# Optimization experiments

Measured on AMD Instinct MI355X. Metric: run time of the kernel, lower is better.

Reference implementation:

```python
import jax, jax.numpy as jnp
import numpy as np

EMBED_DIM = 256
N_HEADS = 1
NORM_FACTOR = float(np.sqrt(EMBED_DIM / N_HEADS))


def setup_inputs() -> dict:
    key = jax.random.key(0)
    ks = jax.random.split(key, 7)
    B, S, E = 4, 4096, EMBED_DIM
    scale = 1.0 / np.sqrt(E)
    x = jax.random.normal(ks[0], (B, S, E), dtype=jnp.float32)
    Wq = jax.random.normal(ks[1], (E, E), dtype=jnp.float32) * scale
    bq = jax.random.normal(ks[2], (E,), dtype=jnp.float32) * 0.01
    Wk = jax.random.normal(ks[3], (E, E), dtype=jnp.float32) * scale
    bk = jax.random.normal(ks[4], (E,), dtype=jnp.float32) * 0.01
    Wv = jax.random.normal(ks[5], (E, E), dtype=jnp.float32) * scale
    bv = jax.random.normal(ks[6], (E,), dtype=jnp.float32) * 0.01
    return {"x": x, "Wq": Wq, "bq": bq, "Wk": Wk, "bk": bk, "Wv": Wv, "bv": bv}


def reference(x, Wq, bq, Wk, bk, Wv, bv):
    # Linear projections (torch Linear: x @ W.T + b; W here stored as [in, out]-equivalent square)
    q = x @ Wq + bq  # [B, S, E]
    k = x @ Wk + bk  # [B, S, E]
    v = x @ Wv + bv  # [B, S, E]
    # Full attention scores [B, S, S], scaled by sqrt(embed_dim / n_heads)
    attn_scores = jnp.einsum('bse,bte->bst', q, k) / NORM_FACTOR
    attn_dist = jax.nn.softmax(attn_scores, axis=-1)
    pooled = jnp.einsum('bst,bte->bse', attn_dist, v)  # [B, S, E]
    return pooled.mean(axis=1, keepdims=True)  # [B, 1, E]
```

## Files before the change

kernel.cpp:

```cpp
#include <hip/hip_runtime.h>
#include <hip/hip_fp8.h>
#include <stdint.h>

#define SS 4096
#define EE 256
#define C2 0.0901684400555602f
#define SCALE1 0x7F7F7F7F
#define ZMAX 8.5f

typedef __bf16 bf16x8 __attribute__((ext_vector_type(8)));
typedef float  f32x4  __attribute__((ext_vector_type(4)));
typedef float  f32x2  __attribute__((ext_vector_type(2)));
typedef int    i32x8  __attribute__((ext_vector_type(8)));

#if __has_builtin(__builtin_amdgcn_exp2f)
#define EXP2(x) __builtin_amdgcn_exp2f(x)
#else
#define EXP2(x) exp2f(x)
#endif
#if __has_builtin(__builtin_amdgcn_rcpf)
#define RCP(x) __builtin_amdgcn_rcpf(x)
#else
#define RCP(x) (1.0f / (x))
#endif

__device__ __forceinline__ uint16_t bf16_rn(float f) {
  uint32_t u = __float_as_uint(f);
  uint32_t r = (u + 0x7fffu + ((u >> 16) & 1u)) >> 16;
  return (uint16_t)r;
}
__device__ __forceinline__ float bf2f(uint16_t h) {
  return __uint_as_float(((uint32_t)h) << 16);
}
__device__ __forceinline__ bf16x8 pack_bf8(float4 a, float4 b) {
  union { bf16x8 v; uint16_t u[8]; } r;
  r.u[0] = bf16_rn(a.x); r.u[1] = bf16_rn(a.y);
  r.u[2] = bf16_rn(a.z); r.u[3] = bf16_rn(a.w);
  r.u[4] = bf16_rn(b.x); r.u[5] = bf16_rn(b.y);
  r.u[6] = bf16_rn(b.z); r.u[7] = bf16_rn(b.w);
  return r.v;
}
__device__ __forceinline__ uint8_t f32_to_e4m3(float x) {
#if __has_builtin(__builtin_amdgcn_cvt_pk_fp8_f32)
  return (uint8_t)(__builtin_amdgcn_cvt_pk_fp8_f32(x, 0.f, 0, false) & 0xff);
#else
  __hip_fp8_e4m3 h(x);
  return (uint8_t)h.__x;
#endif
}
__device__ __forceinline__ uint32_t pack4_e4m3(float a, float b, float c, float d) {
#if __has_builtin(__builtin_amdgcn_cvt_pk_fp8_f32)
  int v = __builtin_amdgcn_cvt_pk_fp8_f32(a, b, 0, false);
  v = __builtin_amdgcn_cvt_pk_fp8_f32(c, d, v, true);
  return (uint32_t)v;
#else
  return (uint32_t)f32_to_e4m3(a) | ((uint32_t)f32_to_e4m3(b) << 8) |
         ((uint32_t)f32_to_e4m3(c) << 16) | ((uint32_t)f32_to_e4m3(d) << 24);
#endif
}
__device__ __forceinline__ float e4m3_f32(uint32_t u) {
  uint32_t bits = ((u & 0x80u) << 24) | ((u & 0x7fu) << 20);
  return __uint_as_float(bits) * 0x1p+120f;
}
__device__ __forceinline__ void decode_fma4(uint32_t w, float rv, float* acc) {
#if __has_builtin(__builtin_amdgcn_cvt_pk_f32_fp8)
  f32x2 lo = __builtin_amdgcn_cvt_pk_f32_fp8((int)w, false);
  f32x2 hi = __builtin_amdgcn_cvt_pk_f32_fp8((int)w, true);
  acc[0] += rv * lo[0]; acc[1] += rv * lo[1];
  acc[2] += rv * hi[0]; acc[3] += rv * hi[1];
#else
  acc[0] += rv * e4m3_f32(w & 0xffu);
  acc[1] += rv * e4m3_f32((w >> 8) & 0xffu);
  acc[2] += rv * e4m3_f32((w >> 16) & 0xffu);
  acc[3] += rv * e4m3_f32(w >> 24);
#endif
}

__device__ __forceinline__ f32x4 mfma16(bf16x8 a, bf16x8 b, f32x4 c) {
  return __builtin_amdgcn_mfma_f32_16x16x32_bf16(a, b, c, 0, 0, 0);
}
__device__ __forceinline__ f32x4 mfma128(i32x8 a, i32x8 b, f32x4 c) {
  return __builtin_amdgcn_mfma_scale_f32_16x16x128_f8f6f4(
      a, b, c, 0 , 0 , 0, SCALE1, 0, SCALE1);
}

template<int R>
__device__ __forceinline__ void stage_tile(const uint16_t* gsrc, char* lds, int tid) {
  constexpr int NPER = (R * 32) / 256;
  const int wave = tid >> 6;
  #pragma unroll
  for (int c = 0; c < NPER; ++c) {
    int chunk = c * 256 + tid;
    int r = chunk >> 5;
    int ccl = (chunk & 31) ^ (r & 31);
    const char* gp = (const char*)gsrc + (r * 32 + ccl) * 16;
    char* lp = lds + (c * 256 + wave * 64) * 16;
    __builtin_amdgcn_global_load_lds(
        (const __attribute__((address_space(1))) uint32_t*)(uintptr_t)gp,
        (__attribute__((address_space(3))) uint32_t*)(uintptr_t)lp,
        16, 0, 0);
  }
}
__device__ __forceinline__ bf16x8 read_frag(const char* lds, int row, int cc) {
  int ccp = cc ^ (row & 31);
  return *(const bf16x8*)(lds + (row * 32 + ccp) * 16);
}

__device__ __forceinline__ void stage_fp8_64(const uint8_t* gsrc, char* lds, int tid) {
  #pragma unroll
  for (int c = 0; c < 4; ++c) {
    int chunk = c * 256 + tid;
    int r = chunk >> 4;
    int ccl = (chunk & 15) ^ (r & 15);
    const char* gp = (const char*)gsrc + (r * 16 + ccl) * 16;
    char* lp = lds + (c * 256 + (tid >> 6) * 64) * 16;
    __builtin_amdgcn_global_load_lds(
        (const __attribute__((address_space(1))) uint32_t*)(uintptr_t)gp,
        (__attribute__((address_space(3))) uint32_t*)(uintptr_t)lp,
        16, 0, 0);
  }
}
__device__ __forceinline__ i32x8 read_frag8(const char* lds, int t, int win, int quad) {
  union { i32x8 v; uint4 q[2]; } r;
  int cc0 = win * 8 + quad * 2;
  r.q[0] = *(const uint4*)(lds + (t * 16 + ((cc0 + 0) ^ (t & 15))) * 16);
  r.q[1] = *(const uint4*)(lds + (t * 16 + ((cc0 + 1) ^ (t & 15))) * 16);
  return r.v;
}

__global__ void prep_kernel(const float* __restrict__ Wq, const float* __restrict__ Wk,
                            const float* __restrict__ Wv, uint16_t* __restrict__ wt,
                            float* __restrict__ zbase, float* __restrict__ out) {
  __shared__ float t[64][65];
  const int bid = blockIdx.x, tid = threadIdx.x;
  if (bid >= 48) {
    int idx = (bid - 48) * 256 + tid;
    float4 z = {0.f, 0.f, 0.f, 0.f};
    if (idx < 8192) ((float4*)zbase)[idx] = z;
    else ((float4*)out)[idx - 8192] = z;
    return;
  }
  const int mat = bid >> 4, tt = bid & 15;
  const int ib = (tt >> 2) * 64, ob = (tt & 3) * 64;
  const float* W = (mat == 0) ? Wq : (mat == 1) ? Wk : Wv;
  #pragma unroll
  for (int p = 0; p < 4; ++p) {
    int idx = p * 256 + tid;
    int r = idx >> 4, c4 = idx & 15;
    float4 f = *(const float4*)&W[(size_t)(ib + r) * 256 + ob + c4 * 4];
    t[r][c4 * 4 + 0] = f.x; t[r][c4 * 4 + 1] = f.y;
    t[r][c4 * 4 + 2] = f.z; t[r][c4 * 4 + 3] = f.w;
  }
  __syncthreads();
  #pragma unroll
  for (int p = 0; p < 4; ++p) {
    int idx = p * 256 + tid;
    int o = idx >> 4, i4 = idx & 15;
    ushort4 u;
    u.x = bf16_rn(t[i4 * 4 + 0][o]);
    u.y = bf16_rn(t[i4 * 4 + 1][o]);
    u.z = bf16_rn(t[i4 * 4 + 2][o]);
    u.w = bf16_rn(t[i4 * 4 + 3][o]);
    *(ushort4*)&wt[((size_t)mat * 256 + ob + o) * 256 + ib + i4 * 4] = u;
  }
}

__global__ __launch_bounds__(256, 2) void qkv_kernel(
    const float* __restrict__ x, const uint16_t* __restrict__ wt,
    const float* __restrict__ bq, const float* __restrict__ bk, const float* __restrict__ bv,
    uint8_t* __restrict__ q8, uint8_t* __restrict__ k8, uint16_t* __restrict__ vo) {
  __shared__ char wsm[2][32768];
  const int tid = threadIdx.x;
  const int lane = tid & 63, wave = tid >> 6, quad = lane >> 4, lr = lane & 15;
  const int m0 = (blockIdx.x >> 2) * 128;
  const int cchunk = blockIdx.x & 3;
  stage_tile<64>(wt + (size_t)(cchunk * 192) * 256, wsm[0], tid);
  const float* ab = x + (size_t)(m0 + wave * 32) * EE;
  bf16x8 a[2][8];
  #pragma unroll
  for (int ms = 0; ms < 2; ++ms)
    #pragma unroll
    for (int f = 0; f < 8; ++f) {
      const float* rp = ab + (size_t)(ms * 16 + lr) * EE + f * 32 + quad * 8;
      a[ms][f] = pack_bf8(*(const float4*)rp, *(const float4*)(rp + 4));
    }
  for (int nc = 0; nc < 3; ++nc) {
    __syncthreads();
    if (nc < 2)
      stage_tile<64>(wt + (size_t)(cchunk * 192 + (nc + 1) * 64) * 256, wsm[(nc + 1) & 1], tid);
    const char* tile = wsm[nc & 1];
    #pragma unroll
    for (int nt = 0; nt < 4; ++nt) {
      const int eg0 = cchunk * 192 + nc * 64 + nt * 16;
      const int mat = eg0 >> 8;
      const int e = (eg0 & 255) + lr;
      const float* bias = (mat == 0) ? bq : (mat == 1) ? bk : bv;
      bf16x8 bf[8];
      #pragma unroll
      for (int f = 0; f < 8; ++f) bf[f] = read_frag(tile, nt * 16 + lr, f * 4 + quad);
      f32x4 acc[2] = {};
      #pragma unroll
      for (int f = 0; f < 8; ++f)
        #pragma unroll
        for (int ms = 0; ms < 2; ++ms)
          acc[ms] = mfma16(a[ms][f], bf[f], acc[ms]);
      const float bsv = bias[e];
      #pragma unroll
      for (int ms = 0; ms < 2; ++ms)
        #pragma unroll
        for (int r = 0; r < 4; ++r) {
          int row = m0 + wave * 32 + ms * 16 + quad * 4 + r;
          float vl = acc[ms][r] + bsv;
          if (mat == 2)      vo[(size_t)row * EE + e] = bf16_rn(vl);
          else if (mat == 1) k8[(size_t)row * EE + e] = f32_to_e4m3(vl);
          else               q8[(size_t)row * EE + e] = f32_to_e4m3(vl);
        }
    }
  }
}

__global__ __launch_bounds__(256, 4) void scores_pl_kernel(
    const uint8_t* __restrict__ q8, const uint8_t* __restrict__ k8,
    uint8_t* __restrict__ p8, float* __restrict__ lacc) {
  __shared__ char qt[2][16384];
  __shared__ float lsh[256];
  const int tid = threadIdx.x;
  const int lane = tid & 63, wave = tid >> 6, quad = lane >> 4, lr = lane & 15;
  const int idx = blockIdx.x;
  const int b = idx >> 8, rem = idx & 255, kblk = rem >> 4, sch = rem & 15;
  const uint8_t* kb = k8 + (size_t)(b * SS + kblk * 256 + wave * 64) * EE;
  const uint8_t* qw = q8 + (size_t)(b * SS + sch * 256) * EE;
  lsh[tid] = 0.f;
  stage_fp8_64(qw, qt[0], tid);
  i32x8 a[4][2];
  #pragma unroll
  for (int ms = 0; ms < 4; ++ms)
    #pragma unroll
    for (int win = 0; win < 2; ++win)
      a[ms][win] = *(const i32x8*)(kb + (size_t)(ms * 16 + lr) * EE + win * 128 + quad * 32);
  const size_t chunkbase = ((size_t)((b * 16 + sch) * 16 + kblk)) << 16;
  uint8_t* pst = p8 + chunkbase + (size_t)(wave * 16) * 1024 + (size_t)lane * 16;
  for (int it = 0; it < 4; ++it) {
    __syncthreads();
    if (it + 1 < 4) stage_fp8_64(qw + (size_t)(it + 1) * 64 * EE, qt[(it + 1) & 1], tid);
    const char* tile = qt[it & 1];
    #pragma unroll
    for (int nt = 0; nt < 4; ++nt) {
      i32x8 bf0 = read_frag8(tile, nt * 16 + lr, 0, quad);
      i32x8 bf1 = read_frag8(tile, nt * 16 + lr, 1, quad);
      f32x4 acc[4] = {};
      #pragma unroll
      for (int ms = 0; ms < 4; ++ms) {
        acc[ms] = mfma128(a[ms][0], bf0, acc[ms]);
        acc[ms] = mfma128(a[ms][1], bf1, acc[ms]);
      }
      const int sloc = it * 64 + nt * 16 + lr;
      float lpart = 0.f;
      uint32_t pw[4];
      #pragma unroll
      for (int ms = 0; ms < 4; ++ms) {
        float e0 = EXP2(fminf(acc[ms][0] * C2, ZMAX));
        float e1 = EXP2(fminf(acc[ms][1] * C2, ZMAX));
        float e2 = EXP2(fminf(acc[ms][2] * C2, ZMAX));
        float e3 = EXP2(fminf(acc[ms][3] * C2, ZMAX));
        lpart += (e0 + e1) + (e2 + e3);
        pw[ms] = pack4_e4m3(e0, e1, e2, e3);
      }
      uint4 w4; w4.x = pw[0]; w4.y = pw[1]; w4.z = pw[2]; w4.w = pw[3];
      *(uint4*)(pst + (size_t)(it * 4 + nt) * 1024) = w4;
      lpart += __shfl_xor(lpart, 16, 64);
      lpart += __shfl_xor(lpart, 32, 64);
      if (quad == 0) atomicAdd(&lsh[sloc], lpart);
    }
  }
  __syncthreads();
  atomicAdd(&lacc[b * SS + sch * 256 + tid], lsh[tid]);
}

__global__ __launch_bounds__(256) void wsum_kernel(
    const uint8_t* __restrict__ p8, const float* __restrict__ lacc,
    float* __restrict__ wacc) {
  __shared__ float rls[256];
  const int tid = threadIdx.x;
  const int idx = blockIdx.x;
  const int b = idx >> 8, rem = idx & 255, kblk = rem >> 4, sch = rem & 15;
  rls[tid] = RCP(lacc[b * SS + sch * 256 + tid]);
  __syncthreads();
  const int lane = tid & 63, wave_w = tid >> 6, lr = tid & 15;
  const size_t chunkbase = ((size_t)((b * 16 + sch) * 16 + kblk)) << 16;
  const uint8_t* pp = p8 + chunkbase + (size_t)(wave_w * 16) * 1024 + (size_t)lane * 16;
  float acc[16];
  #pragma unroll
  for (int i = 0; i < 16; ++i) acc[i] = 0.f;
  #pragma unroll
  for (int itnt = 0; itnt < 16; ++itnt) {
    uint4 pv = *(const uint4*)(pp + (size_t)itnt * 1024);
    float rv = rls[(itnt >> 2) * 64 + (itnt & 3) * 16 + lr];
    decode_fma4(pv.x, rv, acc + 0);
    decode_fma4(pv.y, rv, acc + 4);
    decode_fma4(pv.z, rv, acc + 8);
    decode_fma4(pv.w, rv, acc + 12);
  }
  #pragma unroll
  for (int d = 1; d < 16; d <<= 1)
    #pragma unroll
    for (int i = 0; i < 16; ++i)
      acc[i] += __shfl_xor(acc[i], d, 64);
  if (lr == 0) {
    float* wp = wacc + b * SS + kblk * 256 + wave_w * 64 + (lane >> 4) * 4;
    #pragma unroll
    for (int ms = 0; ms < 4; ++ms)
      #pragma unroll
      for (int r = 0; r < 4; ++r)
        atomicAdd(&wp[ms * 16 + r], acc[ms * 4 + r]);
  }
}

__global__ void pool_kernel(const float* __restrict__ wvec, const uint16_t* __restrict__ v,
                            float* __restrict__ out) {
  __shared__ float red[4][256];
  const int b = blockIdx.x >> 6, tc = blockIdx.x & 63;
  const int tq = threadIdx.x >> 6, eg = threadIdx.x & 63;
  float acc[4] = {0.f, 0.f, 0.f, 0.f};
  const float* wp = wvec + b * SS + tc * 64;
  const uint16_t* vp = v + (size_t)(b * SS + tc * 64) * EE + eg * 4;
  #pragma unroll
  for (int t = 0; t < 16; ++t) {
    int row = t * 4 + tq;
    float wv = wp[row];
    ushort4 x4 = *(const ushort4*)(vp + (size_t)row * EE);
    acc[0] += wv * bf2f(x4.x);
    acc[1] += wv * bf2f(x4.y);
    acc[2] += wv * bf2f(x4.z);
    acc[3] += wv * bf2f(x4.w);
  }
  #pragma unroll
  for (int j = 0; j < 4; ++j) red[tq][eg * 4 + j] = acc[j];
  __syncthreads();
  if (tq == 0) {
    const float inv = 1.0f / 4096.0f;
    #pragma unroll
    for (int j = 0; j < 4; ++j) {
      float s = red[0][eg * 4 + j] + red[1][eg * 4 + j] +
                red[2][eg * 4 + j] + red[3][eg * 4 + j];
      atomicAdd(&out[b * 256 + eg * 4 + j], s * inv);
    }
  }
}

extern "C" void kernel_launch(void* const* d_in, const int* in_sizes, int n_in,
                              void* d_out, int out_size, void* d_ws, size_t ws_size,
                              hipStream_t stream) {
  const float* x  = (const float*)d_in[0];
  const float* Wq = (const float*)d_in[1];
  const float* bq = (const float*)d_in[2];
  const float* Wk = (const float*)d_in[3];
  const float* bk = (const float*)d_in[4];
  const float* Wv = (const float*)d_in[5];
  const float* bv = (const float*)d_in[6];

  char* ws = (char*)d_ws;
  uint8_t*  q8    = (uint8_t*)(ws);
  uint8_t*  k8    = (uint8_t*)(ws + 4194304);
  uint16_t* vb    = (uint16_t*)(ws + 8388608);
  uint16_t* wt    = (uint16_t*)(ws + 16777216);
  float*    l_arr = (float*)(ws + 17170432);
  float*    w_arr = (float*)(ws + 17235968);
  uint8_t*  p8    = (uint8_t*)(ws + 33554432);
  float* out      = (float*)d_out;

  prep_kernel<<<81, 256, 0, stream>>>(Wq, Wk, Wv, wt, l_arr, out);
  qkv_kernel<<<512, 256, 0, stream>>>(x, wt, bq, bk, bv, q8, k8, vb);
  scores_pl_kernel<<<1024, 256, 0, stream>>>(q8, k8, p8, l_arr);
  wsum_kernel<<<1024, 256, 0, stream>>>(p8, l_arr, w_arr);
  pool_kernel<<<256, 256, 0, stream>>>(w_arr, vb, out);
}
```

Baseline: 153.2 us.

## Load Q fragments directly from global memory instead of LDS double buffer

The scores kernel no longer stages Q tiles into a double-buffered LDS area with global_load_lds. Each wave now reads its Q B-fragments straight from global memory (relying on L1/L2 for reuse across the four waves), the per-iteration barriers are dropped, the iteration loop is fully unrolled, and the occupancy hint in launch_bounds is removed. This cuts 32 KB of LDS per block and the synchronisation cost, but each wave now issues redundant global loads for the same Q rows and loses the explicit prefetch overlap.

New measurement: 162.0 us. 5.7% more time.

```diff
diff --git a/kernel.cpp b/kernel.cpp
--- a/kernel.cpp
+++ b/kernel.cpp
@@ -104,28 +104,6 @@
 __device__ __forceinline__ bf16x8 read_frag(const char* lds, int row, int cc) {
   int ccp = cc ^ (row & 31);
   return *(const bf16x8*)(lds + (row * 32 + ccp) * 16);
-}
-
-__device__ __forceinline__ void stage_fp8_64(const uint8_t* gsrc, char* lds, int tid) {
-  #pragma unroll
-  for (int c = 0; c < 4; ++c) {
-    int chunk = c * 256 + tid;
-    int r = chunk >> 4;
-    int ccl = (chunk & 15) ^ (r & 15);
-    const char* gp = (const char*)gsrc + (r * 16 + ccl) * 16;
-    char* lp = lds + (c * 256 + (tid >> 6) * 64) * 16;
-    __builtin_amdgcn_global_load_lds(
-        (const __attribute__((address_space(1))) uint32_t*)(uintptr_t)gp,
-        (__attribute__((address_space(3))) uint32_t*)(uintptr_t)lp,
-        16, 0, 0);
-  }
-}
-__device__ __forceinline__ i32x8 read_frag8(const char* lds, int t, int win, int quad) {
-  union { i32x8 v; uint4 q[2]; } r;
-  int cc0 = win * 8 + quad * 2;
-  r.q[0] = *(const uint4*)(lds + (t * 16 + ((cc0 + 0) ^ (t & 15))) * 16);
-  r.q[1] = *(const uint4*)(lds + (t * 16 + ((cc0 + 1) ^ (t & 15))) * 16);
-  return r.v;
 }
 
 __global__ void prep_kernel(const float* __restrict__ Wq, const float* __restrict__ Wk,
@@ -219,10 +197,9 @@
   }
 }
 
-__global__ __launch_bounds__(256, 4) void scores_pl_kernel(
+__global__ __launch_bounds__(256) void scores_pl_kernel(
     const uint8_t* __restrict__ q8, const uint8_t* __restrict__ k8,
     uint8_t* __restrict__ p8, float* __restrict__ lacc) {
-  __shared__ char qt[2][16384];
   __shared__ float lsh[256];
   const int tid = threadIdx.x;
   const int lane = tid & 63, wave = tid >> 6, quad = lane >> 4, lr = lane & 15;
@@ -231,7 +208,6 @@
   const uint8_t* kb = k8 + (size_t)(b * SS + kblk * 256 + wave * 64) * EE;
   const uint8_t* qw = q8 + (size_t)(b * SS + sch * 256) * EE;
   lsh[tid] = 0.f;
-  stage_fp8_64(qw, qt[0], tid);
   i32x8 a[4][2];
   #pragma unroll
   for (int ms = 0; ms < 4; ++ms)
@@ -240,14 +216,14 @@
       a[ms][win] = *(const i32x8*)(kb + (size_t)(ms * 16 + lr) * EE + win * 128 + quad * 32);
   const size_t chunkbase = ((size_t)((b * 16 + sch) * 16 + kblk)) << 16;
   uint8_t* pst = p8 + chunkbase + (size_t)(wave * 16) * 1024 + (size_t)lane * 16;
+  __syncthreads();
+  #pragma unroll
   for (int it = 0; it < 4; ++it) {
-    __syncthreads();
-    if (it + 1 < 4) stage_fp8_64(qw + (size_t)(it + 1) * 64 * EE, qt[(it + 1) & 1], tid);
-    const char* tile = qt[it & 1];
     #pragma unroll
     for (int nt = 0; nt < 4; ++nt) {
-      i32x8 bf0 = read_frag8(tile, nt * 16 + lr, 0, quad);
-      i32x8 bf1 = read_frag8(tile, nt * 16 + lr, 1, quad);
+      const uint8_t* qrow = qw + (size_t)(it * 64 + nt * 16 + lr) * EE;
+      i32x8 bf0 = *(const i32x8*)(qrow + quad * 32);
+      i32x8 bf1 = *(const i32x8*)(qrow + 128 + quad * 32);
       f32x4 acc[4] = {};
       #pragma unroll
       for (int ms = 0; ms < 4; ++ms) {
```

## Stage K tile in LDS and stream Q from global; split wsum work across two blocks

Applied to the files above, without the earlier changes.

In the scores kernel the roles of Q and K are swapped. The block's whole 256-row K tile is now staged into 64KB of LDS once, and Q fragments are read straight from global memory, which removes the double-buffered per-iteration staging and the barriers inside the loop. LDS use rises to about 64KB and launch bounds drop to 2 blocks per CU, trading occupancy and register-held K fragments for fewer syncs. The wsum kernel is split into twice as many blocks, each handling half the 16 chunks, which adds parallelism at the cost of more atomics and repeated reciprocal loads.

After: 165.0 us. 1.08x slower.

```diff
diff --git a/kernel.cpp b/kernel.cpp
--- a/kernel.cpp
+++ b/kernel.cpp
@@ -219,40 +219,37 @@
   }
 }
 
-__global__ __launch_bounds__(256, 4) void scores_pl_kernel(
+__global__ __launch_bounds__(256, 2) void scores_pl_kernel(
     const uint8_t* __restrict__ q8, const uint8_t* __restrict__ k8,
     uint8_t* __restrict__ p8, float* __restrict__ lacc) {
-  __shared__ char qt[2][16384];
+  __shared__ char kt[4][16384];
   __shared__ float lsh[256];
   const int tid = threadIdx.x;
   const int lane = tid & 63, wave = tid >> 6, quad = lane >> 4, lr = lane & 15;
   const int idx = blockIdx.x;
   const int b = idx >> 8, rem = idx & 255, kblk = rem >> 4, sch = rem & 15;
-  const uint8_t* kb = k8 + (size_t)(b * SS + kblk * 256 + wave * 64) * EE;
+  const uint8_t* kb0 = k8 + (size_t)(b * SS + kblk * 256) * EE;
   const uint8_t* qw = q8 + (size_t)(b * SS + sch * 256) * EE;
   lsh[tid] = 0.f;
-  stage_fp8_64(qw, qt[0], tid);
-  i32x8 a[4][2];
-  #pragma unroll
-  for (int ms = 0; ms < 4; ++ms)
-    #pragma unroll
-    for (int win = 0; win < 2; ++win)
-      a[ms][win] = *(const i32x8*)(kb + (size_t)(ms * 16 + lr) * EE + win * 128 + quad * 32);
+  #pragma unroll
+  for (int w = 0; w < 4; ++w)
+    stage_fp8_64(kb0 + (size_t)w * 64 * EE, kt[w], tid);
+  const char* myt = kt[wave];
   const size_t chunkbase = ((size_t)((b * 16 + sch) * 16 + kblk)) << 16;
   uint8_t* pst = p8 + chunkbase + (size_t)(wave * 16) * 1024 + (size_t)lane * 16;
+  __syncthreads();
+  #pragma unroll
   for (int it = 0; it < 4; ++it) {
-    __syncthreads();
-    if (it + 1 < 4) stage_fp8_64(qw + (size_t)(it + 1) * 64 * EE, qt[(it + 1) & 1], tid);
-    const char* tile = qt[it & 1];
     #pragma unroll
     for (int nt = 0; nt < 4; ++nt) {
-      i32x8 bf0 = read_frag8(tile, nt * 16 + lr, 0, quad);
-      i32x8 bf1 = read_frag8(tile, nt * 16 + lr, 1, quad);
+      const uint8_t* qrow = qw + (size_t)(it * 64 + nt * 16 + lr) * EE;
+      i32x8 bf0 = *(const i32x8*)(qrow + quad * 32);
+      i32x8 bf1 = *(const i32x8*)(qrow + 128 + quad * 32);
       f32x4 acc[4] = {};
       #pragma unroll
       for (int ms = 0; ms < 4; ++ms) {
-        acc[ms] = mfma128(a[ms][0], bf0, acc[ms]);
-        acc[ms] = mfma128(a[ms][1], bf1, acc[ms]);
+        acc[ms] = mfma128(read_frag8(myt, ms * 16 + lr, 0, quad), bf0, acc[ms]);
+        acc[ms] = mfma128(read_frag8(myt, ms * 16 + lr, 1, quad), bf1, acc[ms]);
       }
       const int sloc = it * 64 + nt * 16 + lr;
       float lpart = 0.f;
@@ -283,18 +280,23 @@
   __shared__ float rls[256];
   const int tid = threadIdx.x;
   const int idx = blockIdx.x;
-  const int b = idx >> 8, rem = idx & 255, kblk = rem >> 4, sch = rem & 15;
+  const int b = idx >> 9;
+  const int sch = (idx >> 5) & 15;
+  const int kblk = (idx >> 1) & 15;
+  const int half = idx & 1;
   rls[tid] = RCP(lacc[b * SS + sch * 256 + tid]);
   __syncthreads();
   const int lane = tid & 63, wave_w = tid >> 6, lr = tid & 15;
   const size_t chunkbase = ((size_t)((b * 16 + sch) * 16 + kblk)) << 16;
-  const uint8_t* pp = p8 + chunkbase + (size_t)(wave_w * 16) * 1024 + (size_t)lane * 16;
+  const uint8_t* pp = p8 + chunkbase +
+      (size_t)(wave_w * 16 + half * 8) * 1024 + (size_t)lane * 16;
   float acc[16];
   #pragma unroll
   for (int i = 0; i < 16; ++i) acc[i] = 0.f;
   #pragma unroll
-  for (int itnt = 0; itnt < 16; ++itnt) {
-    uint4 pv = *(const uint4*)(pp + (size_t)itnt * 1024);
+  for (int i = 0; i < 8; ++i) {
+    const int itnt = half * 8 + i;
+    uint4 pv = *(const uint4*)(pp + (size_t)i * 1024);
     float rv = rls[(itnt >> 2) * 64 + (itnt & 3) * 16 + lr];
     decode_fma4(pv.x, rv, acc + 0);
     decode_fma4(pv.y, rv, acc + 4);
@@ -372,6 +374,6 @@
   prep_kernel<<<81, 256, 0, stream>>>(Wq, Wk, Wv, wt, l_arr, out);
   qkv_kernel<<<512, 256, 0, stream>>>(x, wt, bq, bk, bv, q8, k8, vb);
   scores_pl_kernel<<<1024, 256, 0, stream>>>(q8, k8, p8, l_arr);
-  wsum_kernel<<<1024, 256, 0, stream>>>(p8, l_arr, w_arr);
+  wsum_kernel<<<2048, 256, 0, stream>>>(p8, l_arr, w_arr);
   pool_kernel<<<256, 256, 0, stream>>>(w_arr, vb, out);
 }
```
